# Kernel tuning notes

Hardware: AMD Instinct MI355X
Metric: run time of the kernel (lower is better)

## Reference

```python
import jax, jax.numpy as jnp
import numpy as np

B, L, DIN, D = 16, 4096, 64, 64
HA, HL, WIN, NL, K, DFF = 8, 4, 64, 3, 3, 128


def _ln(x, g, b):
    m = x.mean(-1, keepdims=True)
    v = ((x - m) ** 2).mean(-1, keepdims=True)
    return (x - m) * jax.lax.rsqrt(v + 1e-5) * g + b


def _dynamic_conv(x, kernels, w1, b1, w2, b2):
    # x: (B, C, H, 1); kernels: (K, C_out, C_in, 3, 3)
    b, c, h, w = x.shape
    pooled = x.mean(axis=(2, 3))                      # AdaptiveAvgPool2d(1)
    hdn = jax.nn.relu(pooled @ w1.T + b1)             # 1x1 conv C -> C//4
    attn = jax.nn.softmax(hdn @ w2.T + b2, axis=-1)   # (B, K) kernel weights
    kw = kernels.reshape(K * c, c, 3, 3)              # run all K kernels in one conv
    out = jax.lax.conv_general_dilated(x, kw, (1, 1), [(1, 1), (1, 1)],
                                       dimension_numbers=('NCHW', 'OIHW', 'NCHW'))
    out = out.reshape(b, K, c, h, w)
    return jnp.einsum('bkchw,bk->bchw', out, attn)


def _agent_attn(x, wv, bv, an_bias, na_bias):
    # agent_num = 1: a single pooled agent token per sample
    b, n, c = x.shape
    hd = c // HA
    scale = hd ** -0.5
    v = x @ wv + bv
    lepe = v                                          # get_lepe uses the same linear
    qh = x.reshape(b, n, HA, hd).transpose(0, 2, 1, 3)  # (B, HA, L, hd)
    kh = qh
    vh = v.reshape(b, n, HA, hd).transpose(0, 2, 1, 3)
    agent = x.mean(axis=1).reshape(b, HA, 1, hd)      # AdaptiveAvgPool1d(1) over L
    a_attn = jax.nn.softmax(jnp.einsum('bhad,bhnd->bhan', agent * scale, kh) + an_bias, axis=-1)
    agent_v = jnp.einsum('bhan,bhnd->bhad', a_attn, vh)            # (B, HA, 1, hd)
    nb = jnp.swapaxes(na_bias, -1, -2)                              # (HA, L, 1)
    q_attn = jax.nn.softmax(jnp.einsum('bhnd,bhad->bhna', qh * scale, agent) + nb, axis=-1)
    out = jnp.einsum('bhna,bhad->bhnd', q_attn, agent_v)
    return out.transpose(0, 2, 1, 3).reshape(b, n, c) + lepe


def _local_attn(x, wq, bq, wk, bk, wv, bv, wo, bo):
    b, n, d = x.shape
    dk = d // HL
    nw = n // WIN

    def heads(w, bias):
        return (x @ w + bias).reshape(b, nw, WIN, HL, dk).transpose(0, 3, 1, 2, 4)

    q, k, v = heads(wq, bq), heads(wk, bk), heads(wv, bv)
    s = jnp.einsum('bhwid,bhwjd->bhwij', q, k) / (dk ** 0.5)        # per-window scores
    a = jax.nn.softmax(s, axis=-1)
    o = jnp.einsum('bhwij,bhwjd->bhwid', a, v)
    o = o.transpose(0, 2, 3, 1, 4).reshape(b, n, d)
    return o @ wo + bo


def setup_inputs() -> dict:
    key = jax.random.key(0)
    ks = iter(jax.random.split(key, 40))
    nrm = lambda shape, s=0.02: jax.random.normal(next(ks), shape, jnp.float32) * s
    Cr = DIN // 4
    return {
        'x': jax.random.normal(next(ks), (B, L, DIN), jnp.float32),
        'dc_kernels': nrm((3, K, DIN, DIN, 3, 3), 0.05),
        'dc_w1': nrm((3, Cr, DIN)), 'dc_b1': jnp.zeros((3, Cr), jnp.float32),
        'dc_w2': nrm((3, K, Cr)), 'dc_b2': jnp.zeros((3, K), jnp.float32),
        'emb_w': nrm((DIN, D)), 'emb_b': jnp.zeros((D,), jnp.float32),
        'getv_w': nrm((NL, D, D)), 'getv_b': jnp.zeros((NL, D), jnp.float32),
        'an_bias': nrm((NL, HA, 1, L)), 'na_bias': nrm((NL, HA, 1, L)),
        'wq': nrm((NL, D, D)), 'bq': jnp.zeros((NL, D), jnp.float32),
        'wk': nrm((NL, D, D)), 'bk': jnp.zeros((NL, D), jnp.float32),
        'wv': nrm((NL, D, D)), 'bv': jnp.zeros((NL, D), jnp.float32),
        'wo': nrm((NL, D, D)), 'bo': jnp.zeros((NL, D), jnp.float32),
        'ff_w1': nrm((NL, D, DFF)), 'ff_b1': jnp.zeros((NL, DFF), jnp.float32),
        'ff_w2': nrm((NL, DFF, D)), 'ff_b2': jnp.zeros((NL, D), jnp.float32),
        'ln1_g': jnp.ones((NL, D), jnp.float32), 'ln1_b': jnp.zeros((NL, D), jnp.float32),
        'ln2_g': jnp.ones((NL, D), jnp.float32), 'ln2_b': jnp.zeros((NL, D), jnp.float32),
    }


def reference(x, dc_kernels, dc_w1, dc_b1, dc_w2, dc_b2, emb_w, emb_b,
              getv_w, getv_b, an_bias, na_bias,
              wq, bq, wk, bk, wv, bv, wo, bo,
              ff_w1, ff_b1, ff_w2, ff_b2, ln1_g, ln1_b, ln2_g, ln2_b):
    # dynamic multi-kernel convs on (B, C=d_input, H=L, W=1)
    h = x.transpose(0, 2, 1)[..., None]
    for i in range(3):
        h = _dynamic_conv(h, dc_kernels[i], dc_w1[i], dc_b1[i], dc_w2[i], dc_b2[i])
    h = h[..., 0].transpose(0, 2, 1)
    # data embedding (value_linear=True, value_sqrt=False, pos_emb=False)
    h = h @ emb_w + emb_b
    for i in range(NL):
        attn = _agent_attn(h, getv_w[i], getv_b[i], an_bias[i], na_bias[i]) + \
               _local_attn(h, wq[i], bq[i], wk[i], bk[i], wv[i], bv[i], wo[i], bo[i])
        h1 = _ln(h + attn, ln1_g[i], ln1_b[i])
        ffo = jax.nn.relu(h1 @ ff_w1[i] + ff_b1[i]) @ ff_w2[i] + ff_b2[i]
        h = _ln(h1 + ffo, ln2_g[i], ln2_b[i])
    return h
```

## Files before the change

### kernel.cpp

```cpp
#include <hip/hip_runtime.h>

#define BB 16
#define LL 4096
#define DD 64

typedef const float* __restrict__ cfp;
typedef float* __restrict__ fp;
typedef const ushort* __restrict__ cup;
typedef ushort* __restrict__ up;

typedef __attribute__((ext_vector_type(8))) short bf16x8;
typedef __attribute__((ext_vector_type(4))) float f32x4;
#define MFMA16(a, b, c) __builtin_amdgcn_mfma_f32_16x16x32_bf16(a, b, c, 0, 0, 0)

__device__ __forceinline__ f32x4 zf4(){ f32x4 z; z[0]=0.f; z[1]=0.f; z[2]=0.f; z[3]=0.f; return z; }

union frag_u { bf16x8 v; uint2 u2[2]; uint u[4]; };

__device__ __forceinline__ float4 ld4(const float* p){ return *reinterpret_cast<const float4*>(p); }

__device__ __forceinline__ ushort f2bf(float f){
  uint u = __float_as_uint(f);
  return (ushort)((u + 0x7FFFu + ((u >> 16) & 1u)) >> 16);
}
__device__ __forceinline__ float bf2f(ushort u){
  return __uint_as_float(((uint)u) << 16);
}
__device__ __forceinline__ uint packf2(float a, float b){
  return (uint)f2bf(a) | ((uint)f2bf(b) << 16);
}
__device__ __forceinline__ uint2 pack4(float4 v){
  return make_uint2(packf2(v.x, v.y), packf2(v.z, v.w));
}
__device__ __forceinline__ bf16x8 ldfrag(const ushort* p){ return *reinterpret_cast<const bf16x8*>(p); }

__global__ __launch_bounds__(256) void k_pack(cfp wq, cfp wk, cfp wv, cfp getv, cfp wo,
                                              cfp fw1, cfp fw2, cfp embw,
                                              up dst, up dstE) {
  int layer = blockIdx.y;
  int e = blockIdx.x*256 + threadIdx.x;
  if (e >= 36864) {
    int rem = e - 36864;
    int j = rem & 7, lane = (rem >> 3) & 63, rest = rem >> 9;
    int nt = rest & 3, ks = rest >> 2;
    int k = ks*32 + ((lane >> 4) << 3) + j, n = nt*16 + (lane & 15);
    dstE[rem] = f2bf(embw[k*64 + n]);
    return;
  }
  const float* W; int N, rem;
  if (e < 20480) {
    int mm = e >> 12; rem = e & 4095;
    W = (mm==0?wq: mm==1?wk: mm==2?wv: mm==3?getv: wo) + layer*4096; N = 64;
  } else if (e < 28672) {
    rem = e - 20480; W = fw1 + layer*8192; N = 128;
  } else {
    rem = e - 28672; W = fw2 + layer*8192; N = 64;
  }
  int NT = N >> 4;
  int j = rem & 7, lane = (rem >> 3) & 63, rest = rem >> 9;
  int nt = rest % NT, ks = rest / NT;
  int k = ks*32 + ((lane >> 4) << 3) + j, n = nt*16 + (lane & 15);
  dst[(size_t)layer*36864 + e] = f2bf(W[(size_t)k*N + n]);
}

__global__ __launch_bounds__(256) void k_pool_part(cfp h, fp pp) {
  int b = blockIdx.x, gblk = blockIdx.y, t = threadIdx.x;
  int c = t & 63, r = t >> 6;
  const float* base = h + ((size_t)b*LL + (size_t)gblk*256)*64;
  float acc = 0.f;
  for (int l = r; l < 256; l += 4) acc += base[(size_t)l*64 + c];
  __shared__ float red[4][64];
  red[r][c] = acc; __syncthreads();
  if (t < 64) pp[(b*16 + gblk)*64 + t] = red[0][t]+red[1][t]+red[2][t]+red[3][t];
}

__device__ __forceinline__ void tiny_mlp3(int t, const float* __restrict__ pooled,
                                          cfp w1, cfp b1, cfp w2, cfp b2,
                                          float* attn, float* hdn) {
  if (t < 16) {
    float a = b1[t];
    for (int c = 0; c < 64; ++c) a += pooled[c]*w1[t*64 + c];
    hdn[t] = fmaxf(a, 0.f);
  }
  __syncthreads();
  if (t < 3) {
    float a = b2[t];
    for (int j = 0; j < 16; ++j) a += hdn[j]*w2[t*16 + j];
    attn[t] = a;
  }
  __syncthreads();
  if (t == 0) {
    float m = fmaxf(attn[0], fmaxf(attn[1], attn[2]));
    float e0 = __expf(attn[0]-m), e1 = __expf(attn[1]-m), e2 = __expf(attn[2]-m);
    float s = e0+e1+e2;
    attn[0]=e0/s; attn[1]=e1/s; attn[2]=e2/s;
  }
  __syncthreads();
}

__global__ __launch_bounds__(256) void k_prep0(cfp pp, cfp x, cfp dck, fp R0) {
  int b = blockIdx.x, k = blockIdx.y, t = threadIdx.x;
  __shared__ float S[64], e0v[64], e1v[64], em0[64], em1[64];
  __shared__ float redu[3][256];
  const float* xb = x + (size_t)b*LL*64;
  if (t < 64) {
    float s = 0.f;
    for (int g = 0; g < 16; ++g) s += pp[((size_t)b*16 + g)*64 + t];
    S[t] = s;
    e0v[t] = xb[t]; e1v[t] = xb[64 + t];
    em0[t] = xb[(size_t)(LL-2)*64 + t]; em1[t] = xb[(size_t)(LL-1)*64 + t];
  }
  __syncthreads();
  int co = t & 63, q = t >> 6;
  cfp kb = dck + (size_t)k*36864;
  float pS = 0.f, ph0 = 0.f, phm = 0.f;
  for (int ci = q*16; ci < q*16 + 16; ++ci) {
    size_t base = ((size_t)co*64 + ci)*9 + 1;
    float w0 = kb[base], w1 = kb[base+3], w2 = kb[base+6];
    pS  += w0*(S[ci]-em1[ci]) + w1*S[ci] + w2*(S[ci]-e0v[ci]);
    ph0 += w1*e0v[ci] + w2*e1v[ci];
    phm += w0*em0[ci] + w1*em1[ci];
  }
  redu[0][t] = pS; redu[1][t] = ph0; redu[2][t] = phm;
  __syncthreads();
  if (t < 64) {
    R0[((b*3 + 0)*3 + k)*64 + t] = redu[0][t]+redu[0][64+t]+redu[0][128+t]+redu[0][192+t];
    R0[((b*3 + 1)*3 + k)*64 + t] = redu[1][t]+redu[1][64+t]+redu[1][128+t]+redu[1][192+t];
    R0[((b*3 + 2)*3 + k)*64 + t] = redu[2][t]+redu[2][64+t]+redu[2][128+t]+redu[2][192+t];
  }
}

__global__ __launch_bounds__(256) void k_prep1(cfp R0, cfp dck, fp T1) {
  int b = blockIdx.x, k = blockIdx.y / 3, k0 = blockIdx.y % 3, t = threadIdx.x;
  __shared__ float u0[64], u1[64], u2[64];
  __shared__ float redu[256];
  if (t < 64) {
    float rs  = R0[((b*3 + 0)*3 + k0)*64 + t];
    float rh0 = R0[((b*3 + 1)*3 + k0)*64 + t];
    float rhm = R0[((b*3 + 2)*3 + k0)*64 + t];
    u0[t] = rs - rhm; u1[t] = rs; u2[t] = rs - rh0;
  }
  __syncthreads();
  int co = t & 63, q = t >> 6;
  cfp kb = dck + 110592 + (size_t)k*36864;
  float pS = 0.f;
  for (int ci = q*16; ci < q*16 + 16; ++ci) {
    size_t base = ((size_t)co*64 + ci)*9 + 1;
    pS += kb[base]*u0[ci] + kb[base+3]*u1[ci] + kb[base+6]*u2[ci];
  }
  redu[t] = pS;
  __syncthreads();
  if (t < 64)
    T1[((size_t)b*9 + blockIdx.y)*64 + t] = redu[t]+redu[64+t]+redu[128+t]+redu[192+t];
}

__global__ __launch_bounds__(256) void k_attns2(cfp pp, cfp R0, cfp T1,
                                                cfp dcw1, cfp dcb1, cfp dcw2, cfp dcb2,
                                                fp attns) {
  int b = blockIdx.x, t = threadIdx.x;
  __shared__ float pooled[64], hdn[16], attn[3], a0s[3], a1s[3];
  if (t < 64) {
    float s = 0.f;
    for (int g = 0; g < 16; ++g) s += pp[((size_t)b*16 + g)*64 + t];
    pooled[t] = s * (1.f/4096.f);
  }
  __syncthreads();
  tiny_mlp3(t, pooled, dcw1, dcb1, dcw2, dcb2, attn, hdn);
  if (t < 3) { attns[b*9 + t] = attn[t]; a0s[t] = attn[t]; }
  __syncthreads();
  if (t < 64) {
    float sn = a0s[0]*R0[((b*3+0)*3 + 0)*64 + t]
             + a0s[1]*R0[((b*3+0)*3 + 1)*64 + t]
             + a0s[2]*R0[((b*3+0)*3 + 2)*64 + t];
    pooled[t] = sn * (1.f/4096.f);
  }
  __syncthreads();
  tiny_mlp3(t, pooled, dcw1+1024, dcb1+16, dcw2+48, dcb2+3, attn, hdn);
  if (t < 3) { attns[b*9 + 3 + t] = attn[t]; a1s[t] = attn[t]; }
  __syncthreads();
  if (t < 64) {
    float s2 = 0.f;
    #pragma unroll
    for (int k = 0; k < 3; ++k)
      #pragma unroll
      for (int k0 = 0; k0 < 3; ++k0)
        s2 += a1s[k]*a0s[k0]*T1[((size_t)b*9 + k*3 + k0)*64 + t];
    pooled[t] = s2 * (1.f/4096.f);
  }
  __syncthreads();
  tiny_mlp3(t, pooled, dcw1+2048, dcb1+32, dcw2+96, dcb2+6, attn, hdn);
  if (t < 3) attns[b*9 + 6 + t] = attn[t];
}

__global__ __launch_bounds__(256) void k_wefff(cfp attns, cfp dck, up weffB) {
  int b = blockIdx.x, stage = blockIdx.y >> 3, slice = blockIdx.y & 7, t = threadIdx.x;
  float a0 = attns[b*9 + stage*3 + 0];
  float a1 = attns[b*9 + stage*3 + 1];
  float a2 = attns[b*9 + stage*3 + 2];
  cfp kern = dck + (size_t)stage*110592;
  int e0i = slice*1536;
  for (int e = e0i + t; e < e0i + 1536; e += 256) {
    int j = e & 7, lane = (e >> 3) & 63, nt = (e >> 9) & 3, ks = e >> 11;
    int k = ks*32 + ((lane >> 4) << 3) + j;
    int co = nt*16 + (lane & 15);
    int kh = k >> 6, ci = k & 63;
    size_t base = ((size_t)co*64 + ci)*9 + kh*3 + 1;
    float v = a0*kern[base] + a1*kern[base + 36864] + a2*kern[base + 2*36864];
    weffB[((size_t)stage*16 + b)*12288 + e] = f2bf(v);
  }
}

__device__ __forceinline__ void conv_mfma(const ushort* Ts, const ushort* wb,
                                          int band, int lr, int lg, int l, f32x4 acc[4]) {
  #pragma unroll
  for (int nt = 0; nt < 4; ++nt) acc[nt] = zf4();
  #pragma unroll
  for (int ks = 0; ks < 6; ++ks) {
    int k8 = ks*32 + lg*8;
    int kh = k8 >> 6, ci = k8 & 63;
    bf16x8 a = ldfrag(Ts + (band + lr + kh)*72 + ci);
    #pragma unroll
    for (int nt = 0; nt < 4; ++nt)
      acc[nt] = MFMA16(a, ldfrag(wb + ((ks*4+nt)*64 + l)*8), acc[nt]);
  }
}

__global__ __launch_bounds__(256) void k_convF(cfp x, cup weffB, cup wE, cfp embb,
                                               up houtB, fp pp) {
  int b = blockIdx.x, wblk = blockIdx.y, t = threadIdx.x;
  int n0 = wblk*64;
  __shared__ ushort TsA[84*72];
  __shared__ ushort TsB[84*72];
  __shared__ float red[64*17];
  int w = t >> 6, l = t & 63, lr = l & 15, lg = l >> 4;

  for (int idx = t; idx < 1344; idx += 256) {
    int r = idx >> 4, c4 = (idx & 15)*4;
    int g = n0 - 4 + r;
    float4 v = make_float4(0.f,0.f,0.f,0.f);
    if (r >= 1 && r <= 70 && g >= 0 && g < LL) v = ld4(x + ((size_t)b*LL + g)*64 + c4);
    *(uint2*)(TsA + r*72 + c4) = pack4(v);
  }
  for (int idx = t; idx < 32; idx += 256) {
    int r = 82 + (idx >> 4), c4 = (idx & 15)*4;
    *(uint2*)(TsB + r*72 + c4) = make_uint2(0u,0u);
  }
  __syncthreads();

  {
    const ushort* wb = weffB + (size_t)b*12288;
    for (int bi = w; bi < 5; bi += 4) {
      int band = 2 + bi*16;
      f32x4 acc[4];
      conv_mfma(TsA, wb, band - 1, lr, lg, l, acc);
      #pragma unroll
      for (int nt = 0; nt < 4; ++nt)
        #pragma unroll
        for (int reg = 0; reg < 4; ++reg) {
          int row = band + lg*4 + reg;
          int g = n0 - 4 + row;
          float v = (g >= 0 && g < LL) ? acc[nt][reg] : 0.f;
          TsB[row*72 + nt*16 + lr] = f2bf(v);
        }
    }
  }
  __syncthreads();
  {
    const ushort* wb = weffB + (size_t)(16 + b)*12288;
    for (int bi = w; bi < 5; bi += 4) {
      int band = 3 + bi*16;
      f32x4 acc[4];
      conv_mfma(TsB, wb, band - 1, lr, lg, l, acc);
      #pragma unroll
      for (int nt = 0; nt < 4; ++nt)
        #pragma unroll
        for (int reg = 0; reg < 4; ++reg) {
          int row = band + lg*4 + reg;
          int g = n0 - 4 + row;
          float v = (g >= 0 && g < LL) ? acc[nt][reg] : 0.f;
          TsA[row*72 + nt*16 + lr] = f2bf(v);
        }
    }
  }
  __syncthreads();
  {
    const ushort* wb = weffB + (size_t)(32 + b)*12288;
    int band = 4 + w*16;
    f32x4 acc[4];
    conv_mfma(TsA, wb, band - 1, lr, lg, l, acc);
    #pragma unroll
    for (int nt = 0; nt < 4; ++nt)
      #pragma unroll
      for (int reg = 0; reg < 4; ++reg)
        TsB[(band + lg*4 + reg)*72 + nt*16 + lr] = f2bf(acc[nt][reg]);
  }
  __syncthreads();
  {
    int band = 4 + w*16;
    f32x4 ea[4];
    #pragma unroll
    for (int nt = 0; nt < 4; ++nt) ea[nt] = zf4();
    #pragma unroll
    for (int ks = 0; ks < 2; ++ks) {
      bf16x8 a = ldfrag(TsB + (band + lr)*72 + ks*32 + lg*8);
      #pragma unroll
      for (int nt = 0; nt < 4; ++nt)
        ea[nt] = MFMA16(a, ldfrag(wE + ((ks*4+nt)*64 + l)*8), ea[nt]);
    }
    #pragma unroll
    for (int nt = 0; nt < 4; ++nt) {
      int col = nt*16 + lr;
      float bc = embb[col], part = 0.f;
      #pragma unroll
      for (int reg = 0; reg < 4; ++reg) {
        int row = band + lg*4 + reg;
        float y = ea[nt][reg] + bc;
        TsA[row*72 + col] = f2bf(y);
        part += y;
      }
      red[col*17 + w*4 + lg] = part;
    }
  }
  __syncthreads();
  for (int idx = t; idx < 512; idx += 256) {
    int r = idx >> 3, c8 = (idx & 7)*8;
    *(uint4*)(houtB + ((size_t)b*LL + n0 + r)*64 + c8) = *(const uint4*)(TsA + (r+4)*72 + c8);
  }
  if (t < 64) {
    float s = 0.f;
    #pragma unroll
    for (int g = 0; g < 16; ++g) s += red[t*17 + g];
    pp[((size_t)b*64 + wblk)*64 + t] = s;
  }
}

__global__ __launch_bounds__(256) void k_agent2(cup h16, cfp anb, cfp pp,
                                                fp pm, fp pe, fp pw) {
  int b = blockIdx.x, ch = blockIdx.y, t = threadIdx.x;
  int w = t >> 6, l = t & 63;
  __shared__ float means_s[64];
  __shared__ float sc[8][258];
  __shared__ float red4[4][64];
  __shared__ float esp[8][33];
  __shared__ float mcs[8], ess[8];
  __shared__ float wred[4][8][64];
  {
    float acc = 0.f;
    for (int c = w; c < 64; c += 4) acc += pp[((size_t)b*64 + c)*64 + l];
    red4[w][l] = acc;
  }
  __syncthreads();
  if (t < 64) means_s[t] = (red4[0][t]+red4[1][t]+red4[2][t]+red4[3][t])
                           * (1.f/4096.f) * 0.35355339059327373f;
  __syncthreads();
  const ushort* hb = h16 + ((size_t)b*LL + (size_t)ch*256)*64;
  int g8 = l >> 3, k8 = l & 7;
  float ms8[8];
  #pragma unroll
  for (int j = 0; j < 8; ++j) ms8[j] = means_s[k8*8 + j];
  #pragma unroll
  for (int it = 0; it < 8; ++it) {
    int n = w*64 + it*8 + g8;
    uint4 hv = *(const uint4*)(hb + (size_t)n*64 + k8*8);
    float d = bf2f((ushort)(hv.x & 0xffffu))*ms8[0] + bf2f((ushort)(hv.x >> 16))*ms8[1]
            + bf2f((ushort)(hv.y & 0xffffu))*ms8[2] + bf2f((ushort)(hv.y >> 16))*ms8[3]
            + bf2f((ushort)(hv.z & 0xffffu))*ms8[4] + bf2f((ushort)(hv.z >> 16))*ms8[5]
            + bf2f((ushort)(hv.w & 0xffffu))*ms8[6] + bf2f((ushort)(hv.w >> 16))*ms8[7];
    sc[k8][n] = d;
  }
  __syncthreads();
  int hh = t >> 5, j0 = (t & 31) * 8;
  const float* ab = anb + (size_t)hh*LL + ch*256 + j0;
  float loc[8];
  float mx = -1e30f;
  #pragma unroll
  for (int k = 0; k < 8; ++k) {
    loc[k] = sc[hh][j0 + k] + ab[k];
    mx = fmaxf(mx, loc[k]);
  }
  esp[hh][t & 31] = mx;
  __syncthreads();
  if (t < 8) {
    float m = -1e30f;
    for (int k = 0; k < 32; ++k) m = fmaxf(m, esp[t][k]);
    mcs[t] = m;
  }
  __syncthreads();
  {
    float M = mcs[hh], s = 0.f;
    #pragma unroll
    for (int k = 0; k < 8; ++k) {
      float e = __expf(loc[k] - M);
      sc[hh][j0 + k] = e;
      s += e;
    }
    esp[hh][t & 31] = s;
  }
  __syncthreads();
  if (t < 8) {
    float s = 0.f;
    for (int k = 0; k < 32; ++k) s += esp[t][k];
    ess[t] = s;
  }
  float acc8[8] = {};
  for (int i = 0; i < 64; ++i) {
    int n = w*64 + i;
    float xv = bf2f(hb[(size_t)n*64 + l]);
    #pragma unroll
    for (int q = 0; q < 8; ++q) acc8[q] = fmaf(sc[q][n], xv, acc8[q]);
  }
  __syncthreads();
  #pragma unroll
  for (int q = 0; q < 8; ++q) wred[w][q][l] = acc8[q];
  __syncthreads();
  for (int o = t; o < 512; o += 256) {
    int q = o >> 6, ll = o & 63;
    pw[(((size_t)b*16 + ch)*8 + q)*64 + ll] =
        wred[0][q][ll]+wred[1][q][ll]+wred[2][q][ll]+wred[3][q][ll];
  }
  if (t < 8) {
    pe[((size_t)b*16 + ch)*8 + t] = ess[t];
    pm[((size_t)b*16 + ch)*8 + t] = mcs[t];
  }
}

template<bool OUT_BF16>
__global__ __launch_bounds__(256, 4) void k_layer(
    cup h16, cfp pm, cfp pe, cfp pw, cfp getv, cfp getvb, cup wB,
    cfp bq, cfp bk, cfp bv, cfp bo,
    cfp g1, cfp be1, cfp b1, cfp b2, cfp g2, cfp be2,
    fp Y, up Y16, fp pp) {
  __shared__ float smem[10048];
  ushort* HsB  = (ushort*)(smem);
  ushort* Qp   = (ushort*)(smem + 2304);
  ushort* Kp   = (ushort*)(smem + 4864);
  ushort* Vt   = (ushort*)(smem + 7424);
  float*  sums = smem + 9728;
  float*  agvs = smem + 9984;
  float*  wm   = smem + 7424;
  float*  msden= smem + 7944;
  ushort* OB   = (ushort*)(smem + 7424);
  float*  red  = smem + 7424;
  ushort* HidB = (ushort*)(smem + 2304);

  int t = threadIdx.x;
  size_t n0 = (size_t)blockIdx.x*64;
  int b = (int)(n0 >> 12);
  int w = t >> 6, l = t & 63, band = w*16, lr = l & 15, lg = l >> 4;

  #pragma unroll
  for (int it = 0; it < 2; ++it) {
    int idx = it*256 + t, r = idx >> 3, c8 = (idx & 7)*8;
    *(uint4*)(HsB + r*72 + c8) = *(const uint4*)(h16 + (n0 + r)*64 + c8);
  }
  if (t < 8) {
    float M = -1e30f;
    for (int c = 0; c < 16; ++c) M = fmaxf(M, pm[((size_t)b*16+c)*8 + t]);
    float d = 0.f;
    for (int c = 0; c < 16; ++c)
      d += pe[((size_t)b*16+c)*8 + t] * __expf(pm[((size_t)b*16+c)*8 + t] - M);
    msden[t] = M; msden[8+t] = d;
  }
  __syncthreads();
  for (int o = t; o < 512; o += 256) {
    int q = o >> 6, l2 = o & 63;
    float M = msden[q], s = 0.f;
    for (int c = 0; c < 16; ++c)
      s += pw[(((size_t)b*16+c)*8 + q)*64 + l2] * __expf(pm[((size_t)b*16+c)*8 + q] - M);
    wm[q*65 + l2] = s / msden[8+q];
  }
  __syncthreads();
  if (t < 64) {
    int q = t >> 3;
    float a = getvb[t];
    for (int c = 0; c < 64; ++c) a = fmaf(wm[q*65 + c], getv[c*64 + t], a);
    agvs[t] = a;
  }
  __syncthreads();

  f32x4 ka[4], va[4], qa[4], la[4];
  #pragma unroll
  for (int nt = 0; nt < 4; ++nt) {
    ka[nt] = zf4(); va[nt] = zf4(); qa[nt] = zf4(); la[nt] = zf4();
  }
  #pragma unroll
  for (int ks = 0; ks < 2; ++ks) {
    bf16x8 a = ldfrag(HsB + (band + lr)*72 + ks*32 + lg*8);
    #pragma unroll
    for (int nt = 0; nt < 4; ++nt) {
      int fo = ((ks*4 + nt)*64 + l)*8;
      qa[nt] = MFMA16(a, ldfrag(wB + fo),         qa[nt]);
      ka[nt] = MFMA16(a, ldfrag(wB + 4096 + fo),  ka[nt]);
      va[nt] = MFMA16(a, ldfrag(wB + 8192 + fo),  va[nt]);
      la[nt] = MFMA16(a, ldfrag(wB + 12288 + fo), la[nt]);
    }
  }
  #pragma unroll
  for (int nt = 0; nt < 4; ++nt) {
    int col = nt*16 + lr;
    float bkc = bk[col], bvc = bv[col], bqc = bq[col];
    #pragma unroll
    for (int reg = 0; reg < 4; ++reg) {
      int tok = band + 4*lg + reg;
      Kp[nt*1280 + tok*20 + lr] = f2bf(ka[nt][reg] + bkc);
      Qp[nt*1280 + tok*20 + lr] = f2bf((qa[nt][reg] + bqc) * 0.25f);
    }
    int tok0 = band + 4*lg;
    *(uint2*)(Vt + nt*1152 + lr*72 + tok0) =
        make_uint2(packf2(va[nt][0]+bvc, va[nt][1]+bvc),
                   packf2(va[nt][2]+bvc, va[nt][3]+bvc));
  }
  __syncthreads();

  {
    frag_u kaf[4], qbf[4], vbf[4], pf;
    #pragma unroll
    for (int tt = 0; tt < 4; ++tt) {
      kaf[tt].u2[0] = *(const uint2*)(Kp + w*1280 + (tt*16+lr)*20 + lg*4);
      kaf[tt].u[2] = 0; kaf[tt].u[3] = 0;
      qbf[tt].u2[0] = *(const uint2*)(Qp + w*1280 + (tt*16+lr)*20 + lg*4);
      qbf[tt].u[2] = 0; qbf[tt].u[3] = 0;
      vbf[tt].u2[0] = *(const uint2*)(Vt + w*1152 + lr*72 + tt*16 + lg*4);
      vbf[tt].u[2] = 0; vbf[tt].u[3] = 0;
    }
    f32x4 st[4][4];
    #pragma unroll
    for (int kt = 0; kt < 4; ++kt)
      #pragma unroll
      for (int qt = 0; qt < 4; ++qt) {
        f32x4 z = zf4();
        st[kt][qt] = MFMA16(kaf[kt].v, qbf[qt].v, z);
      }
    f32x4 oacc[4];
    #pragma unroll
    for (int qt = 0; qt < 4; ++qt) {
      float M = -1e30f;
      #pragma unroll
      for (int kt = 0; kt < 4; ++kt)
        #pragma unroll
        for (int reg = 0; reg < 4; ++reg) M = fmaxf(M, st[kt][qt][reg]);
      M = fmaxf(M, __shfl_xor(M, 16));
      M = fmaxf(M, __shfl_xor(M, 32));
      float s = 0.f;
      #pragma unroll
      for (int kt = 0; kt < 4; ++kt)
        #pragma unroll
        for (int reg = 0; reg < 4; ++reg) {
          float e = __expf(st[kt][qt][reg] - M);
          st[kt][qt][reg] = e; s += e;
        }
      s += __shfl_xor(s, 16);
      s += __shfl_xor(s, 32);
      if (lg == 0) sums[w*64 + qt*16 + lr] = s;
      oacc[qt] = zf4();
    }
    #pragma unroll
    for (int qt = 0; qt < 4; ++qt)
      #pragma unroll
      for (int kt = 0; kt < 4; ++kt) {
        pf.u[0] = packf2(st[kt][qt][0], st[kt][qt][1]);
        pf.u[1] = packf2(st[kt][qt][2], st[kt][qt][3]);
        pf.u[2] = 0; pf.u[3] = 0;
        oacc[qt] = MFMA16(pf.v, vbf[kt].v, oacc[qt]);
      }
    __syncthreads();
    #pragma unroll
    for (int qt = 0; qt < 4; ++qt)
      #pragma unroll
      for (int reg = 0; reg < 4; ++reg) {
        int q = qt*16 + 4*lg + reg;
        OB[q*72 + band + lr] = f2bf(oacc[qt][reg] / sums[w*64 + q]);
      }
  }
  __syncthreads();

  float comb[4][4];
  {
    f32x4 wa[4];
    #pragma unroll
    for (int nt = 0; nt < 4; ++nt) wa[nt] = zf4();
    #pragma unroll
    for (int ks = 0; ks < 2; ++ks) {
      bf16x8 a = ldfrag(OB + (band + lr)*72 + ks*32 + lg*8);
      #pragma unroll
      for (int nt = 0; nt < 4; ++nt)
        wa[nt] = MFMA16(a, ldfrag(wB + 16384 + ((ks*4+nt)*64 + l)*8), wa[nt]);
    }
    #pragma unroll
    for (int nt = 0; nt < 4; ++nt) {
      int col = nt*16 + lr;
      float cadd = bo[col] + agvs[col] + getvb[col];
      #pragma unroll
      for (int reg = 0; reg < 4; ++reg) {
        int row = band + lg*4 + reg;
        comb[nt][reg] = wa[nt][reg] + la[nt][reg] + cadd + bf2f(HsB[row*72 + col]);
      }
    }
  }
  {
    float mean1[4], rstd1[4];
    #pragma unroll
    for (int reg = 0; reg < 4; ++reg) {
      float s = comb[0][reg]+comb[1][reg]+comb[2][reg]+comb[3][reg];
      float qq = comb[0][reg]*comb[0][reg]+comb[1][reg]*comb[1][reg]
               + comb[2][reg]*comb[2][reg]+comb[3][reg]*comb[3][reg];
      s += __shfl_xor(s,1); qq += __shfl_xor(qq,1);
      s += __shfl_xor(s,2); qq += __shfl_xor(qq,2);
      s += __shfl_xor(s,4); qq += __shfl_xor(qq,4);
      s += __shfl_xor(s,8); qq += __shfl_xor(qq,8);
      float mn = s*0.015625f;
      mean1[reg] = mn;
      rstd1[reg] = rsqrtf(qq*0.015625f - mn*mn + 1e-5f);
    }
    #pragma unroll
    for (int nt = 0; nt < 4; ++nt) {
      int col = nt*16 + lr;
      float gg = g1[col], bb = be1[col];
      #pragma unroll
      for (int reg = 0; reg < 4; ++reg) {
        int row = band + lg*4 + reg;
        float h1 = (comb[nt][reg]-mean1[reg])*rstd1[reg]*gg + bb;
        HsB[row*72 + col] = f2bf(h1);
      }
    }
  }
  __syncthreads();

  {
    f32x4 fa[8];
    #pragma unroll
    for (int nt = 0; nt < 8; ++nt) fa[nt] = zf4();
    #pragma unroll
    for (int ks = 0; ks < 2; ++ks) {
      bf16x8 a = ldfrag(HsB + (band + lr)*72 + ks*32 + lg*8);
      #pragma unroll
      for (int nt = 0; nt < 8; ++nt)
        fa[nt] = MFMA16(a, ldfrag(wB + 20480 + ((ks*8+nt)*64 + l)*8), fa[nt]);
    }
    #pragma unroll
    for (int nt = 0; nt < 8; ++nt) {
      int col = nt*16 + lr;
      float b1c = b1[col];
      #pragma unroll
      for (int reg = 0; reg < 4; ++reg) {
        int row = band + lg*4 + reg;
        HidB[row*136 + col] = f2bf(fmaxf(fa[nt][reg] + b1c, 0.f));
      }
    }
  }
  __syncthreads();

  {
    f32x4 f2[4];
    #pragma unroll
    for (int nt = 0; nt < 4; ++nt) f2[nt] = zf4();
    #pragma unroll
    for (int ks = 0; ks < 4; ++ks) {
      bf16x8 a = ldfrag(HidB + (band + lr)*136 + ks*32 + lg*8);
      #pragma unroll
      for (int nt = 0; nt < 4; ++nt)
        f2[nt] = MFMA16(a, ldfrag(wB + 28672 + ((ks*4+nt)*64 + l)*8), f2[nt]);
    }
    float c2[4][4];
    #pragma unroll
    for (int nt = 0; nt < 4; ++nt) {
      int col = nt*16 + lr;
      float b2c = b2[col];
      #pragma unroll
      for (int reg = 0; reg < 4; ++reg) {
        int row = band + lg*4 + reg;
        c2[nt][reg] = f2[nt][reg] + b2c + bf2f(HsB[row*72 + col]);
      }
    }
    float mean2[4], rstd2[4];
    #pragma unroll
    for (int reg = 0; reg < 4; ++reg) {
      float s = c2[0][reg]+c2[1][reg]+c2[2][reg]+c2[3][reg];
      float qq = c2[0][reg]*c2[0][reg]+c2[1][reg]*c2[1][reg]
               + c2[2][reg]*c2[2][reg]+c2[3][reg]*c2[3][reg];
      s += __shfl_xor(s,1); qq += __shfl_xor(qq,1);
      s += __shfl_xor(s,2); qq += __shfl_xor(qq,2);
      s += __shfl_xor(s,4); qq += __shfl_xor(qq,4);
      s += __shfl_xor(s,8); qq += __shfl_xor(qq,8);
      float mn = s*0.015625f;
      mean2[reg] = mn;
      rstd2[reg] = rsqrtf(qq*0.015625f - mn*mn + 1e-5f);
    }
    __syncthreads();
    #pragma unroll
    for (int nt = 0; nt < 4; ++nt) {
      int col = nt*16 + lr;
      float gg = g2[col], bb = be2[col];
      float part = 0.f;
      #pragma unroll
      for (int reg = 0; reg < 4; ++reg) {
        int row = band + lg*4 + reg;
        float y = (c2[nt][reg]-mean2[reg])*rstd2[reg]*gg + bb;
        if (OUT_BF16) Y16[(n0 + row)*64 + col] = f2bf(y);
        else          Y[(n0 + row)*64 + col] = y;
        part += y;
      }
      red[col*17 + w*4 + lg] = part;
    }
  }
  __syncthreads();
  if (t < 64) {
    float s = 0.f;
    #pragma unroll
    for (int g = 0; g < 16; ++g) s += red[t*17 + g];
    pp[(size_t)blockIdx.x*64 + t] = s;
  }
}

extern "C" void kernel_launch(void* const* d_in, const int* in_sizes, int n_in,
                              void* d_out, int out_size, void* d_ws, size_t ws_size,
                              hipStream_t stream) {
  (void)in_sizes; (void)n_in; (void)out_size; (void)ws_size;
  const float* x    = (const float*)d_in[0];
  const float* dck  = (const float*)d_in[1];
  const float* dcw1 = (const float*)d_in[2];
  const float* dcb1 = (const float*)d_in[3];
  const float* dcw2 = (const float*)d_in[4];
  const float* dcb2 = (const float*)d_in[5];
  const float* embw = (const float*)d_in[6];
  const float* embb = (const float*)d_in[7];
  const float* getvw= (const float*)d_in[8];
  const float* getvb= (const float*)d_in[9];
  const float* anb  = (const float*)d_in[10];
  const float* wq = (const float*)d_in[12]; const float* bq = (const float*)d_in[13];
  const float* wk = (const float*)d_in[14]; const float* bk = (const float*)d_in[15];
  const float* wv = (const float*)d_in[16]; const float* bv = (const float*)d_in[17];
  const float* wo = (const float*)d_in[18]; const float* bo = (const float*)d_in[19];
  const float* fw1= (const float*)d_in[20]; const float* fb1= (const float*)d_in[21];
  const float* fw2= (const float*)d_in[22]; const float* fb2= (const float*)d_in[23];
  const float* g1 = (const float*)d_in[24]; const float* be1= (const float*)d_in[25];
  const float* g2 = (const float*)d_in[26]; const float* be2= (const float*)d_in[27];

  float* out = (float*)d_out;
  float* ws  = (float*)d_ws;
  float* pp    = ws;
  float* pm    = pp + 65536;
  float* pe    = pm + 2048;
  float* pw    = pe + 2048;
  float* attns = pw + 131072;
  float* R0    = attns + 256;
  float* T1    = R0 + 9216;
  ushort* hB0  = (ushort*)(T1 + 9216);
  ushort* hB1  = hB0 + (size_t)BB*LL*64;
  ushort* weffB= hB1 + (size_t)BB*LL*64;
  ushort* wsB  = weffB + (size_t)3*BB*12288;
  ushort* wsE  = wsB + (size_t)3*36864;

  dim3 blk(256);
  const int NT = BB*LL/64;

  k_pack<<<dim3(160, 3), blk, 0, stream>>>(wq, wk, wv, getvw, wo, fw1, fw2, embw, wsB, wsE);
  k_pool_part<<<dim3(BB,16), blk, 0, stream>>>(x, pp);
  k_prep0<<<dim3(BB,3), blk, 0, stream>>>(pp, x, dck, R0);
  k_prep1<<<dim3(BB,9), blk, 0, stream>>>(R0, dck, T1);
  k_attns2<<<BB, blk, 0, stream>>>(pp, R0, T1, dcw1, dcb1, dcw2, dcb2, attns);
  k_wefff<<<dim3(BB,24), blk, 0, stream>>>(attns, dck, weffB);
  k_convF<<<dim3(BB,64), blk, 0, stream>>>(x, weffB, wsE, embb, hB0, pp);

  ushort* h  = hB0;
  ushort* hn = hB1;
  for (int i = 0; i < 3; ++i) {
    k_agent2<<<dim3(BB,16), blk, 0, stream>>>(h, anb + (size_t)i*8*4096, pp, pm, pe, pw);
    if (i == 2) {
      k_layer<false><<<NT, blk, 0, stream>>>(h, pm, pe, pw, getvw + i*4096, getvb + i*64,
                                             wsB + (size_t)i*36864,
                                             bq + i*64, bk + i*64, bv + i*64, bo + i*64,
                                             g1 + i*64, be1 + i*64, fb1 + i*128, fb2 + i*64,
                                             g2 + i*64, be2 + i*64, out, nullptr, pp);
    } else {
      k_layer<true><<<NT, blk, 0, stream>>>(h, pm, pe, pw, getvw + i*4096, getvb + i*64,
                                            wsB + (size_t)i*36864,
                                            bq + i*64, bk + i*64, bv + i*64, bo + i*64,
                                            g1 + i*64, be1 + i*64, fb1 + i*128, fb2 + i*64,
                                            g2 + i*64, be2 + i*64, nullptr, hn, pp);
    }
    ushort* tmp = h; h = hn; hn = tmp;
  }
}
```

Measured before the change: 190.6 us.

## Hoist agent-value finalization into its own kernel and split agent pass finer

Moves the per-sample agent softmax merge and getv projection out of every k_layer block (1024 blocks each redoing it) into a small k_agfin kernel run once per batch. k_agent2 now uses 32 chunks of 128 rows instead of 16 chunks of 256, which doubles its grid. The weight pack and pooling kernels are merged into one launch, and the last layer skips its unused pooled-sum reduction. The cost is one extra launch per layer and a global read of agv inside k_layer.

```diff
diff --git a/kernel.cpp b/kernel.cpp
--- a/kernel.cpp
+++ b/kernel.cpp
@@ -3,6 +3,7 @@
 #define BB 16
 #define LL 4096
 #define DD 64
+#define NCH 32
 
 typedef const float* __restrict__ cfp;
 typedef float* __restrict__ fp;
@@ -34,44 +35,46 @@
 }
 __device__ __forceinline__ bf16x8 ldfrag(const ushort* p){ return *reinterpret_cast<const bf16x8*>(p); }
 
-__global__ __launch_bounds__(256) void k_pack(cfp wq, cfp wk, cfp wv, cfp getv, cfp wo,
-                                              cfp fw1, cfp fw2, cfp embw,
-                                              up dst, up dstE) {
-  int layer = blockIdx.y;
-  int e = blockIdx.x*256 + threadIdx.x;
-  if (e >= 36864) {
-    int rem = e - 36864;
+__global__ __launch_bounds__(256) void k_setup(cfp wq, cfp wk, cfp wv, cfp getv, cfp wo,
+                                               cfp fw1, cfp fw2, cfp embw,
+                                               up dst, up dstE, cfp x, fp pp) {
+  int bx = blockIdx.x, t = threadIdx.x;
+  if (bx < 480) {
+    int layer = bx / 160;
+    int e = (bx % 160)*256 + t;
+    if (e >= 36864) {
+      int rem = e - 36864;
+      int j = rem & 7, lane = (rem >> 3) & 63, rest = rem >> 9;
+      int nt = rest & 3, ks = rest >> 2;
+      int k = ks*32 + ((lane >> 4) << 3) + j, n = nt*16 + (lane & 15);
+      dstE[rem] = f2bf(embw[k*64 + n]);
+      return;
+    }
+    const float* W; int N, rem;
+    if (e < 20480) {
+      int mm = e >> 12; rem = e & 4095;
+      W = (mm==0?wq: mm==1?wk: mm==2?wv: mm==3?getv: wo) + layer*4096; N = 64;
+    } else if (e < 28672) {
+      rem = e - 20480; W = fw1 + layer*8192; N = 128;
+    } else {
+      rem = e - 28672; W = fw2 + layer*8192; N = 64;
+    }
+    int NT = N >> 4;
     int j = rem & 7, lane = (rem >> 3) & 63, rest = rem >> 9;
-    int nt = rest & 3, ks = rest >> 2;
+    int nt = rest % NT, ks = rest / NT;
     int k = ks*32 + ((lane >> 4) << 3) + j, n = nt*16 + (lane & 15);
-    dstE[rem] = f2bf(embw[k*64 + n]);
-    return;
-  }
-  const float* W; int N, rem;
-  if (e < 20480) {
-    int mm = e >> 12; rem = e & 4095;
-    W = (mm==0?wq: mm==1?wk: mm==2?wv: mm==3?getv: wo) + layer*4096; N = 64;
-  } else if (e < 28672) {
-    rem = e - 20480; W = fw1 + layer*8192; N = 128;
+    dst[(size_t)layer*36864 + e] = f2bf(W[(size_t)k*N + n]);
   } else {
-    rem = e - 28672; W = fw2 + layer*8192; N = 64;
-  }
-  int NT = N >> 4;
-  int j = rem & 7, lane = (rem >> 3) & 63, rest = rem >> 9;
-  int nt = rest % NT, ks = rest / NT;
-  int k = ks*32 + ((lane >> 4) << 3) + j, n = nt*16 + (lane & 15);
-  dst[(size_t)layer*36864 + e] = f2bf(W[(size_t)k*N + n]);
-}
-
-__global__ __launch_bounds__(256) void k_pool_part(cfp h, fp pp) {
-  int b = blockIdx.x, gblk = blockIdx.y, t = threadIdx.x;
-  int c = t & 63, r = t >> 6;
-  const float* base = h + ((size_t)b*LL + (size_t)gblk*256)*64;
-  float acc = 0.f;
-  for (int l = r; l < 256; l += 4) acc += base[(size_t)l*64 + c];
-  __shared__ float red[4][64];
-  red[r][c] = acc; __syncthreads();
-  if (t < 64) pp[(b*16 + gblk)*64 + t] = red[0][t]+red[1][t]+red[2][t]+red[3][t];
+    int idx = bx - 480;
+    int b = idx >> 4, gblk = idx & 15;
+    int c = t & 63, r = t >> 6;
+    const float* base = x + ((size_t)b*LL + (size_t)gblk*256)*64;
+    float acc = 0.f;
+    for (int l = r; l < 256; l += 4) acc += base[(size_t)l*64 + c];
+    __shared__ float red[4][64];
+    red[r][c] = acc; __syncthreads();
+    if (t < 64) pp[(b*16 + gblk)*64 + t] = red[0][t]+red[1][t]+red[2][t]+red[3][t];
+  }
 }
 
 __device__ __forceinline__ void tiny_mlp3(int t, const float* __restrict__ pooled,
@@ -339,7 +342,7 @@
   int b = blockIdx.x, ch = blockIdx.y, t = threadIdx.x;
   int w = t >> 6, l = t & 63;
   __shared__ float means_s[64];
-  __shared__ float sc[8][258];
+  __shared__ float sc[8][130];
   __shared__ float red4[4][64];
   __shared__ float esp[8][33];
   __shared__ float mcs[8], ess[8];
@@ -353,14 +356,14 @@
   if (t < 64) means_s[t] = (red4[0][t]+red4[1][t]+red4[2][t]+red4[3][t])
                            * (1.f/4096.f) * 0.35355339059327373f;
   __syncthreads();
-  const ushort* hb = h16 + ((size_t)b*LL + (size_t)ch*256)*64;
+  const ushort* hb = h16 + ((size_t)b*LL + (size_t)ch*128)*64;
   int g8 = l >> 3, k8 = l & 7;
   float ms8[8];
   #pragma unroll
   for (int j = 0; j < 8; ++j) ms8[j] = means_s[k8*8 + j];
   #pragma unroll
-  for (int it = 0; it < 8; ++it) {
-    int n = w*64 + it*8 + g8;
+  for (int it = 0; it < 4; ++it) {
+    int n = w*32 + it*8 + g8;
     uint4 hv = *(const uint4*)(hb + (size_t)n*64 + k8*8);
     float d = bf2f((ushort)(hv.x & 0xffffu))*ms8[0] + bf2f((ushort)(hv.x >> 16))*ms8[1]
             + bf2f((ushort)(hv.y & 0xffffu))*ms8[2] + bf2f((ushort)(hv.y >> 16))*ms8[3]
@@ -369,12 +372,12 @@
     sc[k8][n] = d;
   }
   __syncthreads();
-  int hh = t >> 5, j0 = (t & 31) * 8;
-  const float* ab = anb + (size_t)hh*LL + ch*256 + j0;
-  float loc[8];
+  int hh = t >> 5, j0 = (t & 31) * 4;
+  const float* ab = anb + (size_t)hh*LL + ch*128 + j0;
+  float loc[4];
   float mx = -1e30f;
   #pragma unroll
-  for (int k = 0; k < 8; ++k) {
+  for (int k = 0; k < 4; ++k) {
     loc[k] = sc[hh][j0 + k] + ab[k];
     mx = fmaxf(mx, loc[k]);
   }
@@ -389,7 +392,7 @@
   {
     float M = mcs[hh], s = 0.f;
     #pragma unroll
-    for (int k = 0; k < 8; ++k) {
+    for (int k = 0; k < 4; ++k) {
       float e = __expf(loc[k] - M);
       sc[hh][j0 + k] = e;
       s += e;
@@ -403,8 +406,8 @@
     ess[t] = s;
   }
   float acc8[8] = {};
-  for (int i = 0; i < 64; ++i) {
-    int n = w*64 + i;
+  for (int i = 0; i < 32; ++i) {
+    int n = w*32 + i;
     float xv = bf2f(hb[(size_t)n*64 + l]);
     #pragma unroll
     for (int q = 0; q < 8; ++q) acc8[q] = fmaf(sc[q][n], xv, acc8[q]);
@@ -415,30 +418,57 @@
   __syncthreads();
   for (int o = t; o < 512; o += 256) {
     int q = o >> 6, ll = o & 63;
-    pw[(((size_t)b*16 + ch)*8 + q)*64 + ll] =
+    pw[(((size_t)b*NCH + ch)*8 + q)*64 + ll] =
         wred[0][q][ll]+wred[1][q][ll]+wred[2][q][ll]+wred[3][q][ll];
   }
   if (t < 8) {
-    pe[((size_t)b*16 + ch)*8 + t] = ess[t];
-    pm[((size_t)b*16 + ch)*8 + t] = mcs[t];
+    pe[((size_t)b*NCH + ch)*8 + t] = ess[t];
+    pm[((size_t)b*NCH + ch)*8 + t] = mcs[t];
+  }
+}
+
+__global__ __launch_bounds__(256) void k_agfin(cfp pm, cfp pe, cfp pw,
+                                               cfp getv, cfp getvb, fp agv) {
+  int b = blockIdx.x, t = threadIdx.x;
+  __shared__ float wm[8][65];
+  __shared__ float Ms[8], den[8];
+  if (t < 8) {
+    float M = -1e30f;
+    for (int c = 0; c < NCH; ++c) M = fmaxf(M, pm[((size_t)b*NCH+c)*8 + t]);
+    float d = 0.f;
+    for (int c = 0; c < NCH; ++c)
+      d += pe[((size_t)b*NCH+c)*8 + t] * __expf(pm[((size_t)b*NCH+c)*8 + t] - M);
+    Ms[t] = M; den[t] = d;
+  }
+  __syncthreads();
+  for (int o = t; o < 512; o += 256) {
+    int q = o >> 6, l = o & 63;
+    float M = Ms[q], s = 0.f;
+    for (int c = 0; c < NCH; ++c)
+      s += pw[(((size_t)b*NCH+c)*8 + q)*64 + l] * __expf(pm[((size_t)b*NCH+c)*8 + q] - M);
+    wm[q][l] = s / den[q];
+  }
+  __syncthreads();
+  if (t < 64) {
+    int q = t >> 3;
+    float a = getvb[t];
+    for (int c = 0; c < 64; ++c) a = fmaf(wm[q][c], getv[c*64 + t], a);
+    agv[b*64 + t] = a;
   }
 }
 
 template<bool OUT_BF16>
 __global__ __launch_bounds__(256, 4) void k_layer(
-    cup h16, cfp pm, cfp pe, cfp pw, cfp getv, cfp getvb, cup wB,
+    cup h16, cfp agv, cfp getvb, cup wB,
     cfp bq, cfp bk, cfp bv, cfp bo,
     cfp g1, cfp be1, cfp b1, cfp b2, cfp g2, cfp be2,
     fp Y, up Y16, fp pp) {
-  __shared__ float smem[10048];
+  __shared__ float smem[9984];
   ushort* HsB  = (ushort*)(smem);
   ushort* Qp   = (ushort*)(smem + 2304);
   ushort* Kp   = (ushort*)(smem + 4864);
   ushort* Vt   = (ushort*)(smem + 7424);
   float*  sums = smem + 9728;
-  float*  agvs = smem + 9984;
-  float*  wm   = smem + 7424;
-  float*  msden= smem + 7944;
   ushort* OB   = (ushort*)(smem + 7424);
   float*  red  = smem + 7424;
   ushort* HidB = (ushort*)(smem + 2304);
@@ -452,29 +482,6 @@
   for (int it = 0; it < 2; ++it) {
     int idx = it*256 + t, r = idx >> 3, c8 = (idx & 7)*8;
     *(uint4*)(HsB + r*72 + c8) = *(const uint4*)(h16 + (n0 + r)*64 + c8);
-  }
-  if (t < 8) {
-    float M = -1e30f;
-    for (int c = 0; c < 16; ++c) M = fmaxf(M, pm[((size_t)b*16+c)*8 + t]);
-    float d = 0.f;
-    for (int c = 0; c < 16; ++c)
-      d += pe[((size_t)b*16+c)*8 + t] * __expf(pm[((size_t)b*16+c)*8 + t] - M);
-    msden[t] = M; msden[8+t] = d;
-  }
-  __syncthreads();
-  for (int o = t; o < 512; o += 256) {
-    int q = o >> 6, l2 = o & 63;
-    float M = msden[q], s = 0.f;
-    for (int c = 0; c < 16; ++c)
-      s += pw[(((size_t)b*16+c)*8 + q)*64 + l2] * __expf(pm[((size_t)b*16+c)*8 + q] - M);
-    wm[q*65 + l2] = s / msden[8+q];
-  }
-  __syncthreads();
-  if (t < 64) {
-    int q = t >> 3;
-    float a = getvb[t];
-    for (int c = 0; c < 64; ++c) a = fmaf(wm[q*65 + c], getv[c*64 + t], a);
-    agvs[t] = a;
   }
   __syncthreads();
 
@@ -589,7 +596,7 @@
     #pragma unroll
     for (int nt = 0; nt < 4; ++nt) {
       int col = nt*16 + lr;
-      float cadd = bo[col] + agvs[col] + getvb[col];
+      float cadd = bo[col] + agv[b*64 + col] + getvb[col];
       #pragma unroll
       for (int reg = 0; reg < 4; ++reg) {
         int row = band + lg*4 + reg;
@@ -686,7 +693,7 @@
       mean2[reg] = mn;
       rstd2[reg] = rsqrtf(qq*0.015625f - mn*mn + 1e-5f);
     }
-    __syncthreads();
+    if (OUT_BF16) __syncthreads();
     #pragma unroll
     for (int nt = 0; nt < 4; ++nt) {
       int col = nt*16 + lr;
@@ -700,15 +707,17 @@
         else          Y[(n0 + row)*64 + col] = y;
         part += y;
       }
-      red[col*17 + w*4 + lg] = part;
-    }
-  }
-  __syncthreads();
-  if (t < 64) {
-    float s = 0.f;
-    #pragma unroll
-    for (int g = 0; g < 16; ++g) s += red[t*17 + g];
-    pp[(size_t)blockIdx.x*64 + t] = s;
+      if (OUT_BF16) red[col*17 + w*4 + lg] = part;
+    }
+  }
+  if (OUT_BF16) {
+    __syncthreads();
+    if (t < 64) {
+      float s = 0.f;
+      #pragma unroll
+      for (int g = 0; g < 16; ++g) s += red[t*17 + g];
+      pp[(size_t)blockIdx.x*64 + t] = s;
+    }
   }
 }
 
@@ -740,9 +749,10 @@
   float* ws  = (float*)d_ws;
   float* pp    = ws;
   float* pm    = pp + 65536;
-  float* pe    = pm + 2048;
-  float* pw    = pe + 2048;
-  float* attns = pw + 131072;
+  float* pe    = pm + 4096;
+  float* pw    = pe + 4096;
+  float* agv   = pw + 262144;
+  float* attns = agv + 1024;
   float* R0    = attns + 256;
   float* T1    = R0 + 9216;
   ushort* hB0  = (ushort*)(T1 + 9216);
@@ -754,8 +764,7 @@
   dim3 blk(256);
   const int NT = BB*LL/64;
 
-  k_pack<<<dim3(160, 3), blk, 0, stream>>>(wq, wk, wv, getvw, wo, fw1, fw2, embw, wsB, wsE);
-  k_pool_part<<<dim3(BB,16), blk, 0, stream>>>(x, pp);
+  k_setup<<<736, blk, 0, stream>>>(wq, wk, wv, getvw, wo, fw1, fw2, embw, wsB, wsE, x, pp);
   k_prep0<<<dim3(BB,3), blk, 0, stream>>>(pp, x, dck, R0);
   k_prep1<<<dim3(BB,9), blk, 0, stream>>>(R0, dck, T1);
   k_attns2<<<BB, blk, 0, stream>>>(pp, R0, T1, dcw1, dcb1, dcw2, dcb2, attns);
@@ -765,15 +774,16 @@
   ushort* h  = hB0;
   ushort* hn = hB1;
   for (int i = 0; i < 3; ++i) {
-    k_agent2<<<dim3(BB,16), blk, 0, stream>>>(h, anb + (size_t)i*8*4096, pp, pm, pe, pw);
+    k_agent2<<<dim3(BB,NCH), blk, 0, stream>>>(h, anb + (size_t)i*8*4096, pp, pm, pe, pw);
+    k_agfin<<<BB, blk, 0, stream>>>(pm, pe, pw, getvw + i*4096, getvb + i*64, agv);
     if (i == 2) {
-      k_layer<false><<<NT, blk, 0, stream>>>(h, pm, pe, pw, getvw + i*4096, getvb + i*64,
+      k_layer<false><<<NT, blk, 0, stream>>>(h, agv, getvb + i*64,
                                              wsB + (size_t)i*36864,
                                              bq + i*64, bk + i*64, bv + i*64, bo + i*64,
                                              g1 + i*64, be1 + i*64, fb1 + i*128, fb2 + i*64,
                                              g2 + i*64, be2 + i*64, out, nullptr, pp);
     } else {
-      k_layer<true><<<NT, blk, 0, stream>>>(h, pm, pe, pw, getvw + i*4096, getvb + i*64,
+      k_layer<true><<<NT, blk, 0, stream>>>(h, agv, getvb + i*64,
                                             wsB + (size_t)i*36864,
                                             bq + i*64, bk + i*64, bv + i*64, bo + i*64,
                                             g1 + i*64, be1 + i*64, fb1 + i*128, fb2 + i*64,
```

Measured after the change: 186.0 us, median of 2. 2.4% less time.
